# Kernel optimization log

Measured on AMD Instinct MI355X. Metric: run time of the kernel, lower is better.

The kernel has to match this reference:

```python
import jax, jax.numpy as jnp
import numpy as np

NCTX, RANK, DIM = 32, 64, 8192
ID = 65536
DD_PER = ID // NCTX  # 2048 intrinsic dims per context token
LL = 8192            # next power of two >= DIM (here equal to DIM)


def setup_inputs() -> dict:
    key = jax.random.key(0)
    ks = jax.random.split(key, 8)
    U = jax.random.normal(ks[0], (NCTX, RANK), dtype=jnp.float32)
    s = jax.random.normal(ks[1], (RANK,), dtype=jnp.float32)
    V = jax.random.normal(ks[2], (DD_PER, RANK), dtype=jnp.float32)
    shared_V = jax.random.normal(ks[3], (DD_PER,), dtype=jnp.float32)
    initial = jax.random.normal(ks[4], (NCTX, DIM), dtype=jnp.float32)
    # Rademacher +/-1 diagonal per context token
    BB = jnp.where(jax.random.normal(ks[5], (NCTX, LL)) >= 0, 1.0, -1.0).astype(jnp.float32)
    GG = jax.random.normal(ks[6], (NCTX, LL), dtype=jnp.float32)
    # independent permutation of [0, LL) per context token
    Pi = jnp.argsort(jax.random.uniform(ks[7], (NCTX, LL)), axis=1).astype(jnp.int32)
    return {"U": U, "s": s, "V": V, "shared_V": shared_V,
            "initial": initial, "BB": BB, "GG": GG, "Pi": Pi}


def wht(x):
    """Unnormalized fast Walsh-Hadamard transform over last axis. x: (B, L), L pow2."""
    B, L = x.shape
    h = 1
    while h < L:
        xr = x.reshape(B, L // (2 * h), 2, h)
        a, b = xr[:, :, 0, :], xr[:, :, 1, :]
        x = jnp.stack((a + b, a - b), axis=2).reshape(B, L)
        h *= 2
    return x


def fastfood(x, BB, Pi, GG):
    """Batched fastfood projection: x (nctx, dd) -> (nctx, DIM)."""
    nctx, dd = x.shape
    xp = jnp.pad(x, ((0, 0), (0, LL - dd)))          # pad to LL
    m = wht(xp * BB)                                  # H B x
    m = jnp.take_along_axis(m, Pi, axis=1) * GG       # G Pi H B x
    m = wht(m)                                        # H G Pi H B x
    divisor = jnp.sqrt(LL * jnp.sum(GG * GG, axis=1, keepdims=True))
    return m[:, :DIM] / (divisor * np.sqrt(float(DIM) / LL))


def reference(U, s, V, shared_V, initial, BB, GG, Pi):
    # low-rank reconstruction: (nctx, DD_PER)
    recon = jnp.einsum('lr,r,dr->ld', U, s, V) + shared_V[None, :]
    ray = fastfood(recon, BB, Pi, GG)                 # (nctx, DIM)
    return initial + ray
```

## Files before the change

kernel.cpp:

```cpp
#include <hip/hip_runtime.h>
#include <math.h>

#define NCTXC 32
#define RANKC 64
#define LLC   8192
#define DDC   2048
#define NT    256
#define NPROD 64
#define MAGIC 0x5CA1AB1Eu

__device__ __forceinline__ void bfly(float& a, float& b) {
    float p = a + b, q = a - b;
    a = p; b = q;
}
__device__ __forceinline__ void bfly4(float4& a, float4& b) {
    bfly(a.x, b.x); bfly(a.y, b.y); bfly(a.z, b.z); bfly(a.w, b.w);
}

__global__ __launch_bounds__(NT, 1) void intrinsic_fused_kernel(
    const float* __restrict__ U, const float* __restrict__ s,
    const float* __restrict__ V, const float* __restrict__ sharedV,
    const float* __restrict__ initial, const float* __restrict__ BB,
    const float* __restrict__ GG, const int* __restrict__ Pi,
    float* __restrict__ out, float* __restrict__ x0,
    unsigned int* __restrict__ flags)
{
    const int bid = blockIdx.x;
    const int t   = threadIdx.x;

    if (bid < NPROD) {
        const int d0 = bid * 32;
        const int l  = t >> 3;
        const int i0 = 4 * (t & 7);

        const float4* U4 = (const float4*)U;
        const float4* s4 = (const float4*)s;
        const float4* V4 = (const float4*)V;

        float4 w4[16];
#pragma unroll
        for (int r4 = 0; r4 < 16; ++r4) {
            float4 u = U4[l * 16 + r4];
            float4 sv = s4[r4];
            w4[r4] = make_float4(u.x * sv.x, u.y * sv.y, u.z * sv.z, u.w * sv.w);
        }
        float v[4];
#pragma unroll
        for (int c = 0; c < 4; ++c) {
            const float4* Vr = V4 + (size_t)(d0 + i0 + c) * 16;
            float a = 0.f;
#pragma unroll
            for (int r4 = 0; r4 < 16; ++r4) {
                float4 vv = Vr[r4];
                a += w4[r4].x * vv.x + w4[r4].y * vv.y +
                     w4[r4].z * vv.z + w4[r4].w * vv.w;
            }
            v[c] = a;
        }
        float4 sh = *(const float4*)(sharedV + d0 + i0);
        float4 bb = *(const float4*)(BB + (size_t)l * LLC + d0 + i0);
        v[0] = (v[0] + sh.x) * bb.x;  v[1] = (v[1] + sh.y) * bb.y;
        v[2] = (v[2] + sh.z) * bb.z;  v[3] = (v[3] + sh.w) * bb.w;

        bfly(v[0], v[1]); bfly(v[2], v[3]);
        bfly(v[0], v[2]); bfly(v[1], v[3]);
#pragma unroll
        for (int mi = 0; mi < 3; ++mi) {
            const int m = 1 << mi;
            const float sgn = (t & m) ? -1.f : 1.f;
#pragma unroll
            for (int c = 0; c < 4; ++c) {
                float p = __shfl_xor(v[c], m);
                v[c] = fmaf(sgn, v[c], p);
            }
        }
        *(float4*)(x0 + (size_t)l * DDC + d0 + i0) =
            make_float4(v[0], v[1], v[2], v[3]);

        __syncthreads();
        if (t == 0)
            __hip_atomic_store(&flags[bid], MAGIC, __ATOMIC_RELEASE,
                               __HIP_MEMORY_SCOPE_AGENT);
        return;
    }

    __shared__ __align__(16) float xs[DDC];
    __shared__ __align__(16) float ys[LLC];
    __shared__ float wsum[4];

    const int l = bid - NPROD;

    const int4*   PiP = (const int4*)(Pi + (size_t)l * LLC) + 8 * t;
    const float4* GGP = (const float4*)(GG + (size_t)l * LLC) + 8 * t;
    int4 pi[8]; float4 gg[8];
#pragma unroll
    for (int u = 0; u < 8; ++u) { pi[u] = PiP[u]; gg[u] = GGP[u]; }

    float4 iv[16];
    if (t < 128) {
        const float4* InP = (const float4*)(initial + (size_t)l * LLC);
#pragma unroll
        for (int m = 0; m < 16; ++m) iv[m] = InP[t + 128 * m];
    }

    float gs = 0.f;
#pragma unroll
    for (int u = 0; u < 8; ++u) {
        float4 g = gg[u];
        gs += g.x * g.x + g.y * g.y + g.z * g.z + g.w * g.w;
    }
#pragma unroll
    for (int off = 32; off > 0; off >>= 1) gs += __shfl_down(gs, off);
    if ((t & 63) == 0) wsum[t >> 6] = gs;

    if (t < NPROD)
        while (__hip_atomic_load(&flags[t], __ATOMIC_ACQUIRE,
                                 __HIP_MEMORY_SCOPE_AGENT) != MAGIC) {}
    __syncthreads();

    {
        const float* xrow = x0 + (size_t)l * DDC + (t & 31) + 256 * (t >> 5);
        float r[8];
#pragma unroll
        for (int e = 0; e < 8; ++e) r[e] = xrow[32 * e];
#pragma unroll
        for (int h = 1; h < 8; h <<= 1)
#pragma unroll
            for (int k = 0; k < 8; ++k)
                if (!(k & h)) bfly(r[k], r[k + h]);
        const float sgn = (t & 32) ? -1.f : 1.f;
#pragma unroll
        for (int e = 0; e < 8; ++e) {
            float p = __shfl_xor(r[e], 32);
            r[e] = fmaf(sgn, r[e], p);
        }
        float* xw = xs + (t & 31) + 256 * (t >> 5);
#pragma unroll
        for (int e = 0; e < 8; ++e) xw[32 * e] = r[e];
    }
    __syncthreads();

    {
        float2* xs2 = (float2*)xs;
        float2 g[4];
#pragma unroll
        for (int d = 0; d < 4; ++d) g[d] = xs2[t + 256 * d];
        bfly(g[0].x, g[1].x); bfly(g[2].x, g[3].x);
        bfly(g[0].y, g[1].y); bfly(g[2].y, g[3].y);
        bfly(g[0].x, g[2].x); bfly(g[1].x, g[3].x);
        bfly(g[0].y, g[2].y); bfly(g[1].y, g[3].y);
#pragma unroll
        for (int d = 0; d < 4; ++d) xs2[t + 256 * d] = g[d];
    }
    __syncthreads();

    {
        float r[32];
#pragma unroll
        for (int u = 0; u < 8; ++u) {
            int4 p = pi[u]; float4 g = gg[u];
            r[4*u+0] = xs[p.x & 2047] * g.x;
            r[4*u+1] = xs[p.y & 2047] * g.y;
            r[4*u+2] = xs[p.z & 2047] * g.z;
            r[4*u+3] = xs[p.w & 2047] * g.w;
        }
#pragma unroll
        for (int h = 1; h < 32; h <<= 1)
#pragma unroll
            for (int k = 0; k < 32; ++k)
                if (!(k & h)) bfly(r[k], r[k + h]);
        float4* ys4 = (float4*)ys;
#pragma unroll
        for (int u = 0; u < 8; ++u)
            ys4[8 * t + u] = make_float4(r[4*u], r[4*u+1], r[4*u+2], r[4*u+3]);
    }
    __syncthreads();

    if (t < 128) {
        float4* ys4 = (float4*)ys;
        const int b2 = (t & 7) + 128 * (t >> 3);
        float4 q[16];
#pragma unroll
        for (int n = 0; n < 16; ++n) q[n] = ys4[b2 + 8 * n];
#pragma unroll
        for (int h = 1; h < 16; h <<= 1)
#pragma unroll
            for (int k = 0; k < 16; ++k)
                if (!(k & h)) bfly4(q[k], q[k + h]);
#pragma unroll
        for (int n = 0; n < 16; ++n) ys4[b2 + 8 * n] = q[n];
    }
    __syncthreads();

    if (t < 128) {
        float4* ys4 = (float4*)ys;
        float4 q[16];
#pragma unroll
        for (int m = 0; m < 16; ++m) q[m] = ys4[t + 128 * m];
#pragma unroll
        for (int h = 1; h < 16; h <<= 1)
#pragma unroll
            for (int k = 0; k < 16; ++k)
                if (!(k & h)) bfly4(q[k], q[k + h]);
        const float invd =
            rsqrtf(8192.f * ((wsum[0] + wsum[1]) + (wsum[2] + wsum[3])));
        float4* OutP = (float4*)(out + (size_t)l * LLC);
#pragma unroll
        for (int m = 0; m < 16; ++m) {
            float4 a = iv[m];
            OutP[t + 128 * m] = make_float4(a.x + q[m].x * invd,
                                            a.y + q[m].y * invd,
                                            a.z + q[m].z * invd,
                                            a.w + q[m].w * invd);
        }
    }
}

extern "C" void kernel_launch(void* const* d_in, const int* in_sizes, int n_in,
                              void* d_out, int out_size, void* d_ws, size_t ws_size,
                              hipStream_t stream) {
    const float* U       = (const float*)d_in[0];
    const float* s       = (const float*)d_in[1];
    const float* V       = (const float*)d_in[2];
    const float* sharedV = (const float*)d_in[3];
    const float* initial = (const float*)d_in[4];
    const float* BB      = (const float*)d_in[5];
    const float* GG      = (const float*)d_in[6];
    const int*   Pi      = (const int*)d_in[7];
    float* out = (float*)d_out;

    float*        x0    = (float*)d_ws;
    unsigned int* flags = (unsigned int*)((char*)d_ws + (1 << 20));

    intrinsic_fused_kernel<<<dim3(NPROD + NCTXC), dim3(NT), 0, stream>>>(
        U, s, V, sharedV, initial, BB, GG, Pi, out, x0, flags);
}
```

Baseline: 15.48 us.

## Move WHT butterflies from producers to consumers and relax flag polling

Producer blocks now write only (recon+shared)*BB, and the consumer blocks do the first WHT levels themselves. Consumers read x0 contiguously as float4, run 3 in-register levels, then 6 shuffle levels. The spin-wait now uses relaxed loads with s_sleep, followed by one acquire fence after the barrier, to cut polling traffic. This shortens producers but adds shuffle work on the consumer critical path. The sleep may also add wake-up latency.

Result: faster. 15.10 us (-2.5%).

```diff
diff --git a/kernel.cpp b/kernel.cpp
--- a/kernel.cpp
+++ b/kernel.cpp
@@ -31,7 +31,7 @@
     if (bid < NPROD) {
         const int d0 = bid * 32;
         const int l  = t >> 3;
-        const int i0 = 4 * (t & 7);
+        const int d  = d0 + 4 * (t & 7);
 
         const float4* U4 = (const float4*)U;
         const float4* s4 = (const float4*)s;
@@ -44,39 +44,23 @@
             float4 sv = s4[r4];
             w4[r4] = make_float4(u.x * sv.x, u.y * sv.y, u.z * sv.z, u.w * sv.w);
         }
-        float v[4];
+        float acc[4];
 #pragma unroll
         for (int c = 0; c < 4; ++c) {
-            const float4* Vr = V4 + (size_t)(d0 + i0 + c) * 16;
+            const float4* Vr = V4 + (size_t)(d + c) * 16;
             float a = 0.f;
 #pragma unroll
             for (int r4 = 0; r4 < 16; ++r4) {
-                float4 vv = Vr[r4];
-                a += w4[r4].x * vv.x + w4[r4].y * vv.y +
-                     w4[r4].z * vv.z + w4[r4].w * vv.w;
+                float4 v = Vr[r4];
+                a += w4[r4].x * v.x + w4[r4].y * v.y + w4[r4].z * v.z + w4[r4].w * v.w;
             }
-            v[c] = a;
-        }
-        float4 sh = *(const float4*)(sharedV + d0 + i0);
-        float4 bb = *(const float4*)(BB + (size_t)l * LLC + d0 + i0);
-        v[0] = (v[0] + sh.x) * bb.x;  v[1] = (v[1] + sh.y) * bb.y;
-        v[2] = (v[2] + sh.z) * bb.z;  v[3] = (v[3] + sh.w) * bb.w;
-
-        bfly(v[0], v[1]); bfly(v[2], v[3]);
-        bfly(v[0], v[2]); bfly(v[1], v[3]);
-#pragma unroll
-        for (int mi = 0; mi < 3; ++mi) {
-            const int m = 1 << mi;
-            const float sgn = (t & m) ? -1.f : 1.f;
-#pragma unroll
-            for (int c = 0; c < 4; ++c) {
-                float p = __shfl_xor(v[c], m);
-                v[c] = fmaf(sgn, v[c], p);
-            }
-        }
-        *(float4*)(x0 + (size_t)l * DDC + d0 + i0) =
-            make_float4(v[0], v[1], v[2], v[3]);
-
+            acc[c] = a;
+        }
+        float4 sh = *(const float4*)(sharedV + d);
+        float4 bb = *(const float4*)(BB + (size_t)l * LLC + d);
+        *(float4*)(x0 + (size_t)l * DDC + d) =
+            make_float4((acc[0] + sh.x) * bb.x, (acc[1] + sh.y) * bb.y,
+                        (acc[2] + sh.z) * bb.z, (acc[3] + sh.w) * bb.w);
         __syncthreads();
         if (t == 0)
             __hip_atomic_store(&flags[bid], MAGIC, __ATOMIC_RELEASE,
@@ -114,29 +98,36 @@
     if ((t & 63) == 0) wsum[t >> 6] = gs;
 
     if (t < NPROD)
-        while (__hip_atomic_load(&flags[t], __ATOMIC_ACQUIRE,
-                                 __HIP_MEMORY_SCOPE_AGENT) != MAGIC) {}
-    __syncthreads();
+        while (__hip_atomic_load(&flags[t], __ATOMIC_RELAXED,
+                                 __HIP_MEMORY_SCOPE_AGENT) != MAGIC)
+            __builtin_amdgcn_s_sleep(1);
+    __syncthreads();
+    __builtin_amdgcn_fence(__ATOMIC_ACQUIRE, "agent");
 
     {
-        const float* xrow = x0 + (size_t)l * DDC + (t & 31) + 256 * (t >> 5);
         float r[8];
-#pragma unroll
-        for (int e = 0; e < 8; ++e) r[e] = xrow[32 * e];
+        const float4* xr = (const float4*)(x0 + (size_t)l * DDC) + 2 * t;
+        float4 a0 = xr[0], a1 = xr[1];
+        r[0]=a0.x; r[1]=a0.y; r[2]=a0.z; r[3]=a0.w;
+        r[4]=a1.x; r[5]=a1.y; r[6]=a1.z; r[7]=a1.w;
 #pragma unroll
         for (int h = 1; h < 8; h <<= 1)
 #pragma unroll
             for (int k = 0; k < 8; ++k)
                 if (!(k & h)) bfly(r[k], r[k + h]);
-        const float sgn = (t & 32) ? -1.f : 1.f;
-#pragma unroll
-        for (int e = 0; e < 8; ++e) {
-            float p = __shfl_xor(r[e], 32);
-            r[e] = fmaf(sgn, r[e], p);
-        }
-        float* xw = xs + (t & 31) + 256 * (t >> 5);
-#pragma unroll
-        for (int e = 0; e < 8; ++e) xw[32 * e] = r[e];
+        const int lane = t & 63;
+#pragma unroll
+        for (int mi = 0; mi < 6; ++mi) {
+            const int m = 1 << mi;
+            const float sgn = (lane & m) ? -1.f : 1.f;
+#pragma unroll
+            for (int k = 0; k < 8; ++k) {
+                float p = __shfl_xor(r[k], m);
+                r[k] = fmaf(sgn, r[k], p);
+            }
+        }
+        *(float4*)(xs + 8 * t)     = make_float4(r[0], r[1], r[2], r[3]);
+        *(float4*)(xs + 8 * t + 4) = make_float4(r[4], r[5], r[6], r[7]);
     }
     __syncthreads();
 
```
